# Optimization experiments

Hardware: AMD Instinct MI355X
Metric: run time of the kernel (lower is better)

## Reference

```python
import jax, jax.numpy as jnp
import numpy as np

B, S, D_MODEL, N_HEADS, D_K, D_V = 2, 2048, 1024, 16, 64, 64


def setup_inputs() -> dict:
    key = jax.random.key(0)
    k1, k2, k3, k4, k5, k6, k7 = jax.random.split(key, 7)
    scale = 1.0 / np.sqrt(D_MODEL)
    inputs = {
        "input_Q": jax.random.normal(k1, (B, S, D_MODEL), dtype=jnp.float32),
        "input_K": jax.random.normal(k2, (B, S, D_MODEL), dtype=jnp.float32),
        "input_V": jax.random.normal(k3, (B, S, D_MODEL), dtype=jnp.float32),
        # causal mask: True means position is masked out (matches masked_fill_)
        "attn_mask": jnp.broadcast_to(
            ~jnp.tril(jnp.ones((S, S), dtype=bool)), (B, S, S)
        ),
        "flag": 0,
        "W_Q": jax.random.normal(k4, (D_MODEL, N_HEADS * D_K), dtype=jnp.float32) * scale,
        "W_K": jax.random.normal(k5, (D_MODEL, N_HEADS * D_K), dtype=jnp.float32) * scale,
        "W_V": jax.random.normal(k6, (D_MODEL, N_HEADS * D_V), dtype=jnp.float32) * scale,
        "W_O": jax.random.normal(k7, (N_HEADS * D_V, D_MODEL), dtype=jnp.float32) * scale,
    }
    return inputs


def reference(input_Q, input_K, input_V, attn_mask, flag, W_Q, W_K, W_V, W_O):
    b = input_Q.shape[0]
    # project and split heads: [b, h, s, d]
    Q = (input_Q @ W_Q).reshape(b, -1, N_HEADS, D_K).transpose(0, 2, 1, 3)
    K = (input_K @ W_K).reshape(b, -1, N_HEADS, D_K).transpose(0, 2, 1, 3)
    V = (input_V @ W_V).reshape(b, -1, N_HEADS, D_V).transpose(0, 2, 1, 3)
    # scaled dot-product attention with additive large-negative masking
    scores = jnp.einsum("bhqd,bhkd->bhqk", Q, K) / np.sqrt(D_K).astype(np.float32)
    scores = jnp.where(attn_mask[:, None, :, :], jnp.float32(-1e9), scores)
    attn = jax.nn.softmax(scores, axis=-1)
    context = jnp.einsum("bhqk,bhkd->bhqd", attn, V)  # [b, h, s, d_v]
    context = context.transpose(0, 2, 1, 3).reshape(b, -1, N_HEADS * D_V)
    return context @ W_O
```

## Files before the change

### kernel.cpp

```cpp
#include <hip/hip_runtime.h>

#define DEVINL __device__ __forceinline__

typedef __attribute__((ext_vector_type(8))) short short8;
typedef __attribute__((ext_vector_type(4))) short sh4;
typedef __attribute__((ext_vector_type(4))) float floatx4;

constexpr int S_LEN = 2048;
constexpr int DM    = 1024;
constexpr int NHEAD = 16;
constexpr int DHEAD = 64;
constexpr int BATCH = 2;
constexpr int MROWS = BATCH * S_LEN;
constexpr float LOG2E = 1.44269504f;
constexpr float SM_C1 = 0.125f * LOG2E;
constexpr float SM_C2 = -24.0f * LOG2E;
constexpr int KSTR = 72;
constexpr int VSTR = 70;

#define MFMA16(a, b, c) __builtin_amdgcn_mfma_f32_16x16x16bf16_1k(a, b, c, 0, 0, 0)

DEVINL unsigned short f2bf(float x) {
  union { float f; unsigned u; } un; un.f = x;
  unsigned u = un.u;
  return (unsigned short)((u + 0x7fffu + ((u >> 16) & 1u)) >> 16);
}
DEVINL unsigned short f2bf_fast(float x) {
  union { float f; unsigned u; } un; un.f = x;
  return (unsigned short)((un.u + 0x8000u) >> 16);
}

__global__ __launch_bounds__(256) void conv3_kernel(const float* __restrict__ s0,
                                                    const float* __restrict__ s1,
                                                    const float* __restrict__ s2,
                                                    unsigned short* __restrict__ d0,
                                                    unsigned short* __restrict__ d1,
                                                    unsigned short* __restrict__ d2) {
  const float* s = blockIdx.y == 0 ? s0 : (blockIdx.y == 1 ? s1 : s2);
  unsigned short* d = blockIdx.y == 0 ? d0 : (blockIdx.y == 1 ? d1 : d2);
  int i = (blockIdx.x * 256 + threadIdx.x) * 4;
  float4 v = *(const float4*)(s + i);
  unsigned lo = (unsigned)f2bf(v.x) | ((unsigned)f2bf(v.y) << 16);
  unsigned hi = (unsigned)f2bf(v.z) | ((unsigned)f2bf(v.w) << 16);
  *(uint2*)(d + i) = make_uint2(lo, hi);
}

__global__ __launch_bounds__(256) void trans4_kernel(const float* __restrict__ W0,
                                                     const float* __restrict__ W1,
                                                     const float* __restrict__ W2,
                                                     const float* __restrict__ W3,
                                                     unsigned short* __restrict__ T0,
                                                     unsigned short* __restrict__ T1,
                                                     unsigned short* __restrict__ T2,
                                                     unsigned short* __restrict__ T3) {
  const float* W = blockIdx.z == 0 ? W0 : (blockIdx.z == 1 ? W1 : (blockIdx.z == 2 ? W2 : W3));
  unsigned short* Wt = blockIdx.z == 0 ? T0 : (blockIdx.z == 1 ? T1 : (blockIdx.z == 2 ? T2 : T3));
  __shared__ unsigned short tile[32][33];
  int t = threadIdx.x;
  int c = t & 31, r0 = t >> 5;
  int nB = blockIdx.x * 32, kB = blockIdx.y * 32;
  for (int i = 0; i < 4; ++i) {
    int r = r0 + i * 8;
    tile[r][c] = f2bf(W[(size_t)(kB + r) * DM + nB + c]);
  }
  __syncthreads();
  for (int i = 0; i < 4; ++i) {
    int r = r0 + i * 8;
    Wt[(size_t)(nB + r) * DM + kB + c] = tile[c][r];
  }
}

DEVINL void load_lds16(const unsigned short* g, unsigned short* l) {
  __builtin_amdgcn_global_load_lds((const __attribute__((address_space(1))) unsigned int*)g,
                                   (__attribute__((address_space(3))) unsigned int*)l,
                                   16, 0, 0);
}

template <int MODE>
DEVINL void gemm_body(const unsigned short* __restrict__ A,
                      const unsigned short* __restrict__ Bt,
                      void* __restrict__ Cout) {
  constexpr int K = 1024, N = 1024;
  __shared__ alignas(16) unsigned short As[128 * 32];
  __shared__ alignas(16) unsigned short Bs[128 * 32];
  const int tid  = threadIdx.x;
  const int wave = tid >> 6, lane = tid & 63;
  const int quad = lane >> 4, l16 = lane & 15;
  const int mBase = blockIdx.y * 128, nBase = blockIdx.x * 128;
  const int wm = (wave >> 1) * 64, wn = (wave & 1) * 64;
  const int sr = lane >> 2;
  const int sc = (lane & 3) * 8;
  floatx4 acc[4][4] = {};

  for (int k0 = 0; k0 < K; k0 += 32) {
    __syncthreads();
#pragma unroll
    for (int j = 0; j < 2; ++j) {
      int row = wave * 32 + j * 16 + sr;
      load_lds16(A  + (size_t)(mBase + row) * K + k0 + sc, As + (wave * 32 + j * 16) * 32);
      load_lds16(Bt + (size_t)(nBase + row) * K + k0 + sc, Bs + (wave * 32 + j * 16) * 32);
    }
    __syncthreads();
    short8 af[4], bfr[4];
#pragma unroll
    for (int mt = 0; mt < 4; ++mt) af[mt]  = *(const short8*)&As[(wm + mt * 16 + l16) * 32 + quad * 8];
#pragma unroll
    for (int nt = 0; nt < 4; ++nt) bfr[nt] = *(const short8*)&Bs[(wn + nt * 16 + l16) * 32 + quad * 8];
#pragma unroll
    for (int mt = 0; mt < 4; ++mt)
#pragma unroll
      for (int nt = 0; nt < 4; ++nt)
        acc[mt][nt] = __builtin_amdgcn_mfma_f32_16x16x32_bf16(af[mt], bfr[nt], acc[mt][nt], 0, 0, 0);
  }

#pragma unroll
  for (int mt = 0; mt < 4; ++mt)
#pragma unroll
    for (int nt = 0; nt < 4; ++nt) {
      const int m = mBase + wm + mt * 16 + quad * 4;
      const int n = nBase + wn + nt * 16 + l16;
      if (MODE == 2) {
        const int bq = m >> 11, s = m & 2047;
        const int hh = n >> 6,  d = n & 63;
        unsigned short w4[4];
#pragma unroll
        for (int r = 0; r < 4; ++r) w4[r] = f2bf(acc[mt][nt][r]);
        *(uint2*)&((unsigned short*)Cout)[((size_t)((bq * 16 + hh) * 64 + d)) * S_LEN + s] =
            *(const uint2*)w4;
      } else {
#pragma unroll
        for (int r = 0; r < 4; ++r) {
          if (MODE == 0) ((unsigned short*)Cout)[(size_t)(m + r) * N + n] = f2bf(acc[mt][nt][r]);
          else           ((float*)Cout)[(size_t)(m + r) * N + n]          = acc[mt][nt][r];
        }
      }
    }
}

__global__ __launch_bounds__(256) void gemm_qkv(const unsigned short* __restrict__ A0,
                                                const unsigned short* __restrict__ A1,
                                                const unsigned short* __restrict__ A2,
                                                const unsigned short* __restrict__ B0,
                                                const unsigned short* __restrict__ B1,
                                                const unsigned short* __restrict__ B2,
                                                unsigned short* __restrict__ C0,
                                                unsigned short* __restrict__ C1,
                                                unsigned short* __restrict__ C2) {
  const int z = blockIdx.z;
  if (z == 2)      gemm_body<2>(A2, B2, C2);
  else if (z == 1) gemm_body<0>(A1, B1, C1);
  else             gemm_body<0>(A0, B0, C0);
}

__global__ __launch_bounds__(256) void gemm_out64(const unsigned short* __restrict__ A,
                                                  const unsigned short* __restrict__ Bt,
                                                  float* __restrict__ C) {
  constexpr int K = 1024, N = 1024;
  __shared__ alignas(16) unsigned short As[64 * 32];
  __shared__ alignas(16) unsigned short Bs[128 * 32];
  const int tid  = threadIdx.x;
  const int wave = tid >> 6, lane = tid & 63;
  const int quad = lane >> 4, l16 = lane & 15;
  const int mBase = blockIdx.y * 64, nBase = blockIdx.x * 128;
  const int wm = (wave >> 1) * 32, wn = (wave & 1) * 64;
  const int sr = lane >> 2;
  const int sc = (lane & 3) * 8;
  floatx4 acc[2][4] = {};

  for (int k0 = 0; k0 < K; k0 += 32) {
    __syncthreads();
    load_lds16(A + (size_t)(mBase + wave * 16 + sr) * K + k0 + sc, As + (wave * 16) * 32);
#pragma unroll
    for (int j = 0; j < 2; ++j) {
      int row = wave * 32 + j * 16 + sr;
      load_lds16(Bt + (size_t)(nBase + row) * K + k0 + sc, Bs + (wave * 32 + j * 16) * 32);
    }
    __syncthreads();
    short8 af[2], bfr[4];
#pragma unroll
    for (int mt = 0; mt < 2; ++mt) af[mt]  = *(const short8*)&As[(wm + mt * 16 + l16) * 32 + quad * 8];
#pragma unroll
    for (int nt = 0; nt < 4; ++nt) bfr[nt] = *(const short8*)&Bs[(wn + nt * 16 + l16) * 32 + quad * 8];
#pragma unroll
    for (int mt = 0; mt < 2; ++mt)
#pragma unroll
      for (int nt = 0; nt < 4; ++nt)
        acc[mt][nt] = __builtin_amdgcn_mfma_f32_16x16x32_bf16(af[mt], bfr[nt], acc[mt][nt], 0, 0, 0);
  }

#pragma unroll
  for (int mt = 0; mt < 2; ++mt)
#pragma unroll
    for (int nt = 0; nt < 4; ++nt)
#pragma unroll
      for (int r = 0; r < 4; ++r) {
        int m = mBase + wm + mt * 16 + quad * 4 + r;
        int n = nBase + wn + nt * 16 + l16;
        C[(size_t)m * N + n] = acc[mt][nt][r];
      }
}

__global__ __launch_bounds__(256, 3) void attn_kernel(const unsigned short* __restrict__ Qp,
                                                      const unsigned short* __restrict__ Kp,
                                                      const unsigned short* __restrict__ Vtg,
                                                      unsigned short* __restrict__ ctx) {
  const int bh = blockIdx.y;
  const int b  = bh >> 4, h = bh & 15;
  const int tid = threadIdx.x;
  const int w = tid >> 6, lane = tid & 63;
  const int quad = lane >> 4, l16 = lane & 15;

  __shared__ alignas(16) unsigned short Ks[64 * KSTR];
  __shared__ alignas(16) unsigned short Vs[64 * VSTR];
  __shared__ float rsL[4][4][16];
  __shared__ alignas(16) float Ored[4][4][16][16];

  const unsigned short* Kbh = Kp  + (size_t)(b * S_LEN) * DM + h * DHEAD;
  const unsigned short* Vbh = Vtg + (size_t)(bh * DHEAD) * S_LEN;

  const int sr = tid >> 3, sc8 = (tid & 7) * 8;
  const unsigned short* kg = Kbh + (size_t)sr * DM + sc8;
  const unsigned short* vg = Vbh + (size_t)sr * S_LEN + sc8;
  unsigned short* ksl = Ks + sr * KSTR + sc8;
  unsigned short* vsl = Vs + sr * VSTR + sc8;

  uint4 kr0 = *(const uint4*)kg;
  uint4 kr1 = *(const uint4*)(kg + (size_t)32 * DM);
  uint4 vr0 = *(const uint4*)vg;
  uint4 vr1 = *(const uint4*)(vg + (size_t)32 * S_LEN);

#pragma unroll 1
  for (int half = 0; half < 2; ++half) {
    const int qt = half ? (int)blockIdx.x : 31 - (int)blockIdx.x;
    const int Q0 = qt * 64;
    const int nT = qt + 1;

    short8 qB[4][2];
#pragma unroll
    for (int nt = 0; nt < 4; ++nt) {
      const size_t qr = ((size_t)(b * S_LEN + Q0 + nt * 16 + l16)) * DM + h * DHEAD + quad * 8;
      qB[nt][0] = *(const short8*)&Qp[qr];
      qB[nt][1] = *(const short8*)&Qp[qr + 32];
    }

    floatx4 o[4][4] = {};
    float rs[4] = {0.f, 0.f, 0.f, 0.f};

#pragma unroll 1
    for (int t = 0; t < nT; ++t) {
      __syncthreads();
      *(uint4*)ksl               = kr0;
      *(uint4*)(ksl + 32 * KSTR) = kr1;
      *(uint4*)vsl               = vr0;
      *(uint4*)(vsl + 32 * VSTR) = vr1;
      __syncthreads();

      if (t + 1 < nT) {
        const int kbn = (t + 1) * 64;
        kr0 = *(const uint4*)(kg + (size_t)kbn * DM);
        kr1 = *(const uint4*)(kg + (size_t)(kbn + 32) * DM);
        vr0 = *(const uint4*)(vg + kbn);
        vr1 = *(const uint4*)(vg + (size_t)32 * S_LEN + kbn);
      } else if (half == 0) {
        kr0 = *(const uint4*)kg;
        kr1 = *(const uint4*)(kg + (size_t)32 * DM);
        vr0 = *(const uint4*)vg;
        vr1 = *(const uint4*)(vg + (size_t)32 * S_LEN);
      }

      short8 kc0 = *(const short8*)&Ks[(w * 16 + l16) * KSTR + quad * 8];
      short8 kc1 = *(const short8*)&Ks[(w * 16 + l16) * KSTR + 32 + quad * 8];
      sh4 vv[4];
#pragma unroll
      for (int dt = 0; dt < 4; ++dt)
        vv[dt] = *(const sh4*)&Vs[(dt * 16 + l16) * VSTR + w * 16 + quad * 4];

      const bool masked = (t == nT - 1);
      const int sbase = w * 16 + quad * 4;

#pragma unroll
      for (int nt = 0; nt < 4; ++nt) {
        floatx4 sc = {};
        sc = __builtin_amdgcn_mfma_f32_16x16x32_bf16(kc0, qB[nt][0], sc, 0, 0, 0);
        sc = __builtin_amdgcn_mfma_f32_16x16x32_bf16(kc1, qB[nt][1], sc, 0, 0, 0);
        const int qoff = nt * 16 + l16;
        sh4 pa;
        float acc = 0.f;
#pragma unroll
        for (int r = 0; r < 4; ++r) {
          float p = __builtin_amdgcn_exp2f(fmaf(sc[r], SM_C1, SM_C2));
          if (masked && (sbase + r > qoff)) p = 0.f;
          acc += p;
          pa[r] = (short)f2bf_fast(p);
        }
        rs[nt] += acc;
#pragma unroll
        for (int dt = 0; dt < 4; ++dt)
          o[nt][dt] = MFMA16(pa, vv[dt], o[nt][dt]);
      }
    }

#pragma unroll
    for (int nt = 0; nt < 4; ++nt) {
      rs[nt] += __shfl_xor(rs[nt], 16, 64);
      rs[nt] += __shfl_xor(rs[nt], 32, 64);
    }
    if (quad == 0) {
#pragma unroll
      for (int nt = 0; nt < 4; ++nt) rsL[w][nt][l16] = rs[nt];
    }

    for (int nt = 0; nt < 4; ++nt) {
      __syncthreads();
#pragma unroll
      for (int dt = 0; dt < 4; ++dt)
        *(floatx4*)&Ored[w][dt][l16][quad * 4] = o[nt][dt];
      __syncthreads();
      floatx4 acc = {};
#pragma unroll
      for (int w2 = 0; w2 < 4; ++w2) {
        floatx4 v = *(const floatx4*)&Ored[w2][w][l16][quad * 4];
#pragma unroll
        for (int j = 0; j < 4; ++j) acc[j] += v[j];
      }
#pragma unroll
      for (int j = 0; j < 4; ++j) {
        const int q16 = quad * 4 + j;
        float l = rsL[0][nt][q16] + rsL[1][nt][q16] + rsL[2][nt][q16] + rsL[3][nt][q16];
        const size_t row = (size_t)(b * S_LEN + Q0 + nt * 16 + q16);
        ctx[row * DM + h * DHEAD + w * 16 + l16] = f2bf(acc[j] / l);
      }
    }
  }
}

extern "C" void kernel_launch(void* const* d_in, const int* in_sizes, int n_in,
                              void* d_out, int out_size, void* d_ws, size_t ws_size,
                              hipStream_t stream) {
  const float* Xq = (const float*)d_in[0];
  const float* Xk = (const float*)d_in[1];
  const float* Xv = (const float*)d_in[2];
  const float* Wq = (const float*)d_in[5];
  const float* Wk = (const float*)d_in[6];
  const float* Wv = (const float*)d_in[7];
  const float* Wo = (const float*)d_in[8];
  float* out = (float*)d_out;

  char* ws = (char*)d_ws;
  constexpr size_t XBYTES = (size_t)MROWS * DM * 2;
  constexpr size_t WBYTES = (size_t)DM * DM * 2;
  unsigned short* xq_bf = (unsigned short*)(ws);
  unsigned short* xk_bf = (unsigned short*)(ws + XBYTES);
  unsigned short* xv_bf = (unsigned short*)(ws + 2 * XBYTES);
  unsigned short* wqt   = (unsigned short*)(ws + 3 * XBYTES);
  unsigned short* wkt   = (unsigned short*)(ws + 3 * XBYTES + WBYTES);
  unsigned short* wvt   = (unsigned short*)(ws + 3 * XBYTES + 2 * WBYTES);
  unsigned short* wot   = (unsigned short*)(ws + 3 * XBYTES + 3 * WBYTES);
  unsigned short* qp    = (unsigned short*)(ws + 3 * XBYTES + 4 * WBYTES);
  unsigned short* kp    = (unsigned short*)(ws + 4 * XBYTES + 4 * WBYTES);
  unsigned short* vt    = (unsigned short*)(ws + 5 * XBYTES + 4 * WBYTES);
  unsigned short* ctx   = xq_bf;

  const int nX = MROWS * DM;
  conv3_kernel<<<dim3(nX / 1024, 3), 256, 0, stream>>>(Xq, Xk, Xv, xq_bf, xk_bf, xv_bf);
  trans4_kernel<<<dim3(32, 32, 4), 256, 0, stream>>>(Wq, Wk, Wv, Wo, wqt, wkt, wvt, wot);

  gemm_qkv<<<dim3(DM / 128, MROWS / 128, 3), 256, 0, stream>>>(
      xq_bf, xk_bf, xv_bf, wqt, wkt, wvt, qp, kp, vt);

  attn_kernel<<<dim3(16, BATCH * NHEAD), 256, 0, stream>>>(qp, kp, vt, ctx);

  gemm_out64<<<dim3(DM / 128, MROWS / 64), 256, 0, stream>>>(ctx, wot, out);
}
```

Baseline: 240.6 us.

## Load attention K/V fragments directly from global and merge prep kernels

The attention kernel drops the shared-memory staging of K and V tiles and the two barriers per key tile. Each wave now loads its own MFMA fragments straight from global memory, prefetching the next tile into registers. Separately, the bf16 conversion and weight transpose kernels are merged into one launch to save a kernel launch. Direct loads use narrower, less coalesced accesses (especially the 8-byte V reads), which may add global/L2 traffic.

```diff
diff --git a/kernel.cpp b/kernel.cpp
--- a/kernel.cpp
+++ b/kernel.cpp
@@ -15,8 +15,6 @@
 constexpr float LOG2E = 1.44269504f;
 constexpr float SM_C1 = 0.125f * LOG2E;
 constexpr float SM_C2 = -24.0f * LOG2E;
-constexpr int KSTR = 72;
-constexpr int VSTR = 70;
 
 #define MFMA16(a, b, c) __builtin_amdgcn_mfma_f32_16x16x16bf16_1k(a, b, c, 0, 0, 0)
 
@@ -30,43 +28,47 @@
   return (unsigned short)((un.u + 0x8000u) >> 16);
 }
 
-__global__ __launch_bounds__(256) void conv3_kernel(const float* __restrict__ s0,
-                                                    const float* __restrict__ s1,
-                                                    const float* __restrict__ s2,
-                                                    unsigned short* __restrict__ d0,
-                                                    unsigned short* __restrict__ d1,
-                                                    unsigned short* __restrict__ d2) {
-  const float* s = blockIdx.y == 0 ? s0 : (blockIdx.y == 1 ? s1 : s2);
-  unsigned short* d = blockIdx.y == 0 ? d0 : (blockIdx.y == 1 ? d1 : d2);
-  int i = (blockIdx.x * 256 + threadIdx.x) * 4;
-  float4 v = *(const float4*)(s + i);
-  unsigned lo = (unsigned)f2bf(v.x) | ((unsigned)f2bf(v.y) << 16);
-  unsigned hi = (unsigned)f2bf(v.z) | ((unsigned)f2bf(v.w) << 16);
-  *(uint2*)(d + i) = make_uint2(lo, hi);
-}
-
-__global__ __launch_bounds__(256) void trans4_kernel(const float* __restrict__ W0,
-                                                     const float* __restrict__ W1,
-                                                     const float* __restrict__ W2,
-                                                     const float* __restrict__ W3,
-                                                     unsigned short* __restrict__ T0,
-                                                     unsigned short* __restrict__ T1,
-                                                     unsigned short* __restrict__ T2,
-                                                     unsigned short* __restrict__ T3) {
-  const float* W = blockIdx.z == 0 ? W0 : (blockIdx.z == 1 ? W1 : (blockIdx.z == 2 ? W2 : W3));
-  unsigned short* Wt = blockIdx.z == 0 ? T0 : (blockIdx.z == 1 ? T1 : (blockIdx.z == 2 ? T2 : T3));
+__global__ __launch_bounds__(256) void prep_kernel(const float* __restrict__ s0,
+                                                   const float* __restrict__ s1,
+                                                   const float* __restrict__ s2,
+                                                   unsigned short* __restrict__ d0,
+                                                   unsigned short* __restrict__ d1,
+                                                   unsigned short* __restrict__ d2,
+                                                   const float* __restrict__ W0,
+                                                   const float* __restrict__ W1,
+                                                   const float* __restrict__ W2,
+                                                   const float* __restrict__ W3,
+                                                   unsigned short* __restrict__ T0,
+                                                   unsigned short* __restrict__ T1,
+                                                   unsigned short* __restrict__ T2,
+                                                   unsigned short* __restrict__ T3) {
   __shared__ unsigned short tile[32][33];
-  int t = threadIdx.x;
-  int c = t & 31, r0 = t >> 5;
-  int nB = blockIdx.x * 32, kB = blockIdx.y * 32;
-  for (int i = 0; i < 4; ++i) {
-    int r = r0 + i * 8;
-    tile[r][c] = f2bf(W[(size_t)(kB + r) * DM + nB + c]);
-  }
-  __syncthreads();
-  for (int i = 0; i < 4; ++i) {
-    int r = r0 + i * 8;
-    Wt[(size_t)(nB + r) * DM + kB + c] = tile[c][r];
+  const int y = blockIdx.y;
+  if (y < 3) {
+    const float* s = y == 0 ? s0 : (y == 1 ? s1 : s2);
+    unsigned short* d = y == 0 ? d0 : (y == 1 ? d1 : d2);
+    int i = (blockIdx.x * 256 + threadIdx.x) * 4;
+    float4 v = *(const float4*)(s + i);
+    unsigned lo = (unsigned)f2bf(v.x) | ((unsigned)f2bf(v.y) << 16);
+    unsigned hi = (unsigned)f2bf(v.z) | ((unsigned)f2bf(v.w) << 16);
+    *(uint2*)(d + i) = make_uint2(lo, hi);
+  } else {
+    const int x = blockIdx.x;
+    const int wsel = x >> 10, rem = x & 1023;
+    const float* W = wsel == 0 ? W0 : (wsel == 1 ? W1 : (wsel == 2 ? W2 : W3));
+    unsigned short* Wt = wsel == 0 ? T0 : (wsel == 1 ? T1 : (wsel == 2 ? T2 : T3));
+    int t = threadIdx.x;
+    int c = t & 31, r0 = t >> 5;
+    int nB = (rem & 31) * 32, kB = (rem >> 5) * 32;
+    for (int i = 0; i < 4; ++i) {
+      int r = r0 + i * 8;
+      tile[r][c] = f2bf(W[(size_t)(kB + r) * DM + nB + c]);
+    }
+    __syncthreads();
+    for (int i = 0; i < 4; ++i) {
+      int r = r0 + i * 8;
+      Wt[(size_t)(nB + r) * DM + kB + c] = tile[c][r];
+    }
   }
 }
 
@@ -210,24 +212,21 @@
   const int w = tid >> 6, lane = tid & 63;
   const int quad = lane >> 4, l16 = lane & 15;
 
-  __shared__ alignas(16) unsigned short Ks[64 * KSTR];
-  __shared__ alignas(16) unsigned short Vs[64 * VSTR];
   __shared__ float rsL[4][4][16];
   __shared__ alignas(16) float Ored[4][4][16][16];
 
   const unsigned short* Kbh = Kp  + (size_t)(b * S_LEN) * DM + h * DHEAD;
   const unsigned short* Vbh = Vtg + (size_t)(bh * DHEAD) * S_LEN;
 
-  const int sr = tid >> 3, sc8 = (tid & 7) * 8;
-  const unsigned short* kg = Kbh + (size_t)sr * DM + sc8;
-  const unsigned short* vg = Vbh + (size_t)sr * S_LEN + sc8;
-  unsigned short* ksl = Ks + sr * KSTR + sc8;
-  unsigned short* vsl = Vs + sr * VSTR + sc8;
-
-  uint4 kr0 = *(const uint4*)kg;
-  uint4 kr1 = *(const uint4*)(kg + (size_t)32 * DM);
-  uint4 vr0 = *(const uint4*)vg;
-  uint4 vr1 = *(const uint4*)(vg + (size_t)32 * S_LEN);
+  const unsigned short* kf = Kbh + (size_t)(w * 16 + l16) * DM + quad * 8;
+  const unsigned short* vf = Vbh + (size_t)l16 * S_LEN + w * 16 + quad * 4;
+
+  short8 kc0 = *(const short8*)kf;
+  short8 kc1 = *(const short8*)(kf + 32);
+  sh4 vv[4];
+#pragma unroll
+  for (int dt = 0; dt < 4; ++dt)
+    vv[dt] = *(const sh4*)(vf + (size_t)(dt * 16) * S_LEN);
 
 #pragma unroll 1
   for (int half = 0; half < 2; ++half) {
@@ -248,32 +247,14 @@
 
 #pragma unroll 1
     for (int t = 0; t < nT; ++t) {
-      __syncthreads();
-      *(uint4*)ksl               = kr0;
-      *(uint4*)(ksl + 32 * KSTR) = kr1;
-      *(uint4*)vsl               = vr0;
-      *(uint4*)(vsl + 32 * VSTR) = vr1;
-      __syncthreads();
-
-      if (t + 1 < nT) {
-        const int kbn = (t + 1) * 64;
-        kr0 = *(const uint4*)(kg + (size_t)kbn * DM);
-        kr1 = *(const uint4*)(kg + (size_t)(kbn + 32) * DM);
-        vr0 = *(const uint4*)(vg + kbn);
-        vr1 = *(const uint4*)(vg + (size_t)32 * S_LEN + kbn);
-      } else if (half == 0) {
-        kr0 = *(const uint4*)kg;
-        kr1 = *(const uint4*)(kg + (size_t)32 * DM);
-        vr0 = *(const uint4*)vg;
-        vr1 = *(const uint4*)(vg + (size_t)32 * S_LEN);
-      }
-
-      short8 kc0 = *(const short8*)&Ks[(w * 16 + l16) * KSTR + quad * 8];
-      short8 kc1 = *(const short8*)&Ks[(w * 16 + l16) * KSTR + 32 + quad * 8];
-      sh4 vv[4];
+      const int tn = (t + 1 < nT) ? t + 1 : 0;
+      const size_t ko = (size_t)tn * 64 * DM;
+      short8 nk0 = *(const short8*)(kf + ko);
+      short8 nk1 = *(const short8*)(kf + ko + 32);
+      sh4 nv[4];
 #pragma unroll
       for (int dt = 0; dt < 4; ++dt)
-        vv[dt] = *(const sh4*)&Vs[(dt * 16 + l16) * VSTR + w * 16 + quad * 4];
+        nv[dt] = *(const sh4*)(vf + (size_t)(dt * 16) * S_LEN + tn * 64);
 
       const bool masked = (t == nT - 1);
       const int sbase = w * 16 + quad * 4;
@@ -298,6 +279,11 @@
         for (int dt = 0; dt < 4; ++dt)
           o[nt][dt] = MFMA16(pa, vv[dt], o[nt][dt]);
       }
+
+      kc0 = nk0;
+      kc1 = nk1;
+#pragma unroll
+      for (int dt = 0; dt < 4; ++dt) vv[dt] = nv[dt];
     }
 
 #pragma unroll
@@ -361,9 +347,8 @@
   unsigned short* vt    = (unsigned short*)(ws + 5 * XBYTES + 4 * WBYTES);
   unsigned short* ctx   = xq_bf;
 
-  const int nX = MROWS * DM;
-  conv3_kernel<<<dim3(nX / 1024, 3), 256, 0, stream>>>(Xq, Xk, Xv, xq_bf, xk_bf, xv_bf);
-  trans4_kernel<<<dim3(32, 32, 4), 256, 0, stream>>>(Wq, Wk, Wv, Wo, wqt, wkt, wvt, wot);
+  prep_kernel<<<dim3(4096, 4), 256, 0, stream>>>(Xq, Xk, Xv, xq_bf, xk_bf, xv_bf,
+                                                 Wq, Wk, Wv, Wo, wqt, wkt, wvt, wot);
 
   gemm_qkv<<<dim3(DM / 128, MROWS / 128, 3), 256, 0, stream>>>(
       xq_bf, xk_bf, xv_bf, wqt, wkt, wvt, qp, kp, vt);
```

After: 247.2 us. +2.8%, slower.
